# Performance work log

Measured on AMD Instinct MI355X. Metric: run time of the kernel, lower is better.

The kernel has to match this reference:

```python
import jax, jax.numpy as jnp
import numpy as np

T, B, V, E, H, L = 128, 32, 50000, 512, 512, 2


def _lstm_layer(x, h0, c0, Wih, Whh, bih, bhh):
    # x: [T, B, in]; torch gate order i, f, g, o
    def step(carry, xt):
        h, c = carry
        gates = xt @ Wih.T + bih + h @ Whh.T + bhh  # [B, 4H]
        i, f, g, o = jnp.split(gates, 4, axis=-1)
        c = jax.nn.sigmoid(f) * c + jax.nn.sigmoid(i) * jnp.tanh(g)
        h = jax.nn.sigmoid(o) * jnp.tanh(c)
        return (h, c), h
    (h, c), ys = jax.lax.scan(step, (h0, c0), x)
    return ys, h, c


def setup_inputs() -> dict:
    key = jax.random.key(0)
    ks = jax.random.split(key, 12)
    s = 0.02
    return {
        'word': jax.random.randint(ks[0], (B,), 0, V),
        'seq': jax.random.randint(ks[1], (T, B), 0, V),
        'emb': jax.random.normal(ks[2], (V, E), jnp.float32) * s,
        'w2h_W': jax.random.normal(ks[3], (H, E), jnp.float32) * s,
        'w2h_b': jnp.zeros((H,), jnp.float32),
        'Wih0': jax.random.normal(ks[4], (4 * H, E), jnp.float32) * s,
        'Whh0': jax.random.normal(ks[5], (4 * H, H), jnp.float32) * s,
        'bih0': jnp.zeros((4 * H,), jnp.float32),
        'bhh0': jnp.zeros((4 * H,), jnp.float32),
        'Wih1': jax.random.normal(ks[6], (4 * H, H), jnp.float32) * s,
        'Whh1': jax.random.normal(ks[7], (4 * H, H), jnp.float32) * s,
        'bih1': jnp.zeros((4 * H,), jnp.float32),
        'bhh1': jnp.zeros((4 * H,), jnp.float32),
        'dec_W': jax.random.normal(ks[8], (V, H), jnp.float32) * s,
        'dec_b': jnp.zeros((V,), jnp.float32),
    }


def reference(word, seq, emb, w2h_W, w2h_b, Wih0, Whh0, bih0, bhh0,
              Wih1, Whh1, bih1, bhh1, dec_W, dec_b):
    word_emb = emb[word]                       # [B, E]
    seq_emb = emb[seq]                         # [T, B, E] (dropouts are 0/eval)
    # init_hidden: c0 = word2hidden(word_emb) expanded to all layers, h0 = 0
    c0 = word_emb @ w2h_W.T + w2h_b            # [B, H]
    h0 = jnp.zeros_like(c0)
    # 2-layer LSTM; stepping all layers per timestep == running layers sequentially
    y0, h_f0, c_f0 = _lstm_layer(seq_emb, h0, c0, Wih0, Whh0, bih0, bhh0)
    y1, h_f1, c_f1 = _lstm_layer(y0, h0, c0, Wih1, Whh1, bih1, bhh1)
    out = y1.reshape(T * B, H)                 # [T*B, H]
    decoded = out @ dec_W.T + dec_b            # [T*B, V]
    h_final = jnp.stack([h_f0, h_f1], axis=0)  # [L, B, H]
    c_final = jnp.stack([c_f0, c_f1], axis=0)
    return decoded, h_final, c_final
```

## Files before the change

kernel.cpp:

```cpp
#include <hip/hip_runtime.h>
#include <hip/hip_bf16.h>
#include <cstdint>

#define T_STEPS 128
#define BATCH   32
#define VOCAB   50000
#define EDIM    512
#define HDIM    512
#define GDIM    2048
#define MROWS   4096
#define VPAD    50048

typedef short bf16x8 __attribute__((ext_vector_type(8)));
typedef float f32x4  __attribute__((ext_vector_type(4)));
typedef unsigned short us4 __attribute__((ext_vector_type(4)));
typedef unsigned short us8 __attribute__((ext_vector_type(8)));

__device__ __forceinline__ float sigmoidf_(float x) { return 1.0f / (1.0f + expf(-x)); }

__device__ __forceinline__ unsigned short f2bf(float f) {
    unsigned int u = __float_as_uint(f);
    u = (u + 0x7fffu + ((u >> 16) & 1u)) >> 16;
    return (unsigned short)u;
}


__global__ __launch_bounds__(256) void conv_decw(const float* __restrict__ src,
                                                 unsigned short* __restrict__ dst) {
    long i = ((long)blockIdx.x * 256 + threadIdx.x) * 8;
    if (i >= (long)VPAD * EDIM) return;
    long row = i >> 9;
    us8 v;
    if (row < VOCAB) {
        float4 a = *(const float4*)(src + i);
        float4 b = *(const float4*)(src + i + 4);
        v[0] = f2bf(a.x); v[1] = f2bf(a.y); v[2] = f2bf(a.z); v[3] = f2bf(a.w);
        v[4] = f2bf(b.x); v[5] = f2bf(b.y); v[6] = f2bf(b.z); v[7] = f2bf(b.w);
    } else {
        v = (us8)0;
    }
    *(us8*)(dst + i) = v;
}

__global__ __launch_bounds__(64) void pack_conv(const float* __restrict__ src,
                                                unsigned short* __restrict__ dst) {
    const int n = blockIdx.x;
    const int orig = (n & 3) * 512 + (n >> 2);
    const int k = threadIdx.x * 8;
    const float* s = src + (long)orig * 512 + k;
    float4 a = *(const float4*)s;
    float4 b = *(const float4*)(s + 4);
    us8 v;
    v[0] = f2bf(a.x); v[1] = f2bf(a.y); v[2] = f2bf(a.z); v[3] = f2bf(a.w);
    v[4] = f2bf(b.x); v[5] = f2bf(b.y); v[6] = f2bf(b.z); v[7] = f2bf(b.w);
    *(us8*)(dst + (long)n * 512 + k) = v;
}

__global__ __launch_bounds__(256) void pack_bias(const float* __restrict__ bih0,
                                                 const float* __restrict__ bhh0,
                                                 const float* __restrict__ bih1,
                                                 const float* __restrict__ bhh1,
                                                 float* __restrict__ b0p,
                                                 float* __restrict__ b1p) {
    const int n = blockIdx.x * 256 + threadIdx.x;
    const int orig = (n & 3) * 512 + (n >> 2);
    b0p[n] = bih0[orig] + bhh0[orig];
    b1p[n] = bih1[orig] + bhh1[orig];
}

__global__ __launch_bounds__(256) void gather_x(const int* __restrict__ seq,
                                                const float* __restrict__ emb,
                                                unsigned short* __restrict__ Xbf) {
    long i = ((long)blockIdx.x * 256 + threadIdx.x) * 4;
    if (i >= (long)MROWS * EDIM) return;
    int r   = (int)(i >> 9);
    int col = (int)(i & 511);
    const float* er = emb + (long)seq[r] * EDIM + col;
    float4 e = *(const float4*)er;
    us4 v;
    v[0] = f2bf(e.x); v[1] = f2bf(e.y); v[2] = f2bf(e.z); v[3] = f2bf(e.w);
    *(us4*)(Xbf + i) = v;
}

__global__ __launch_bounds__(256) void init_c0(const int* __restrict__ word,
                                               const float* __restrict__ emb,
                                               const float* __restrict__ w2hW,
                                               const float* __restrict__ w2hb,
                                               float* __restrict__ c0s, float* __restrict__ c1s,
                                               unsigned short* __restrict__ h0A,
                                               unsigned short* __restrict__ h1A) {
    const int idx = blockIdx.x * 256 + threadIdx.x;
    const int b = idx >> 9, hh = idx & 511;
    const float* er = emb + (long)word[b] * EDIM;
    const float* wr = w2hW + (long)hh * EDIM;
    float acc = w2hb[hh];
    #pragma unroll 4
    for (int k = 0; k < EDIM; k += 4) {
        float4 e4 = *(const float4*)(er + k);
        float4 w4 = *(const float4*)(wr + k);
        acc += e4.x * w4.x + e4.y * w4.y + e4.z * w4.z + e4.w * w4.w;
    }
    c0s[idx] = acc;
    c1s[idx] = acc;
    h0A[idx] = 0;
    h1A[idx] = 0;
}

__global__ __launch_bounds__(256) void gemm_bt128(const unsigned short* __restrict__ A,
                                                  const unsigned short* __restrict__ Bt,
                                                  float* __restrict__ C,
                                                  const float* __restrict__ bias1,
                                                  const float* __restrict__ bias2,
                                                  int K, int Nreal, long ldc, int ntn,
                                                  int ntstore) {
    __shared__ __align__(16) unsigned short As[128 * 64];
    __shared__ __align__(16) unsigned short Bs[128 * 64];
    const int tid  = threadIdx.x;
    const long m0  = (long)(blockIdx.x / ntn) * 128;
    const long n0  = (long)(blockIdx.x % ntn) * 128;
    const int lane = tid & 63;
    const int wave = tid >> 6;
    const int wr = wave >> 1, wc = wave & 1;
    const int fr = lane & 15, fq = lane >> 4;

    f32x4 acc[4][4];
    #pragma unroll
    for (int i = 0; i < 4; ++i)
        #pragma unroll
        for (int j = 0; j < 4; ++j) acc[i][j] = (f32x4)0.0f;

    const int srow = tid >> 3;
    const int scol = (tid & 7) * 8;

    for (int kt = 0; kt < K; kt += 64) {
        #pragma unroll
        for (int i = 0; i < 4; ++i) {
            const unsigned short* ga = A  + (m0 + i * 32 + srow) * K + kt + scol;
            const unsigned short* gb = Bt + (n0 + i * 32 + srow) * K + kt + scol;
            __builtin_amdgcn_global_load_lds((const __attribute__((address_space(1))) void*)ga,
                                             (__attribute__((address_space(3))) void*)(As + i * 2048 + tid * 8),
                                             16, 0, 0);
            __builtin_amdgcn_global_load_lds((const __attribute__((address_space(1))) void*)gb,
                                             (__attribute__((address_space(3))) void*)(Bs + i * 2048 + tid * 8),
                                             16, 0, 0);
        }
        asm volatile("s_waitcnt vmcnt(0)" ::: "memory");
        __syncthreads();
        #pragma unroll
        for (int ks = 0; ks < 64; ks += 32) {
            bf16x8 af[4], bfr[4];
            #pragma unroll
            for (int mi = 0; mi < 4; ++mi)
                af[mi] = *(const bf16x8*)&As[(wr * 64 + mi * 16 + fr) * 64 + ks + fq * 8];
            #pragma unroll
            for (int ni = 0; ni < 4; ++ni)
                bfr[ni] = *(const bf16x8*)&Bs[(wc * 64 + ni * 16 + fr) * 64 + ks + fq * 8];
            #pragma unroll
            for (int mi = 0; mi < 4; ++mi)
                #pragma unroll
                for (int ni = 0; ni < 4; ++ni)
                    acc[mi][ni] = __builtin_amdgcn_mfma_f32_16x16x32_bf16(af[mi], bfr[ni], acc[mi][ni], 0, 0, 0);
        }
        __syncthreads();
    }

    #pragma unroll
    for (int mi = 0; mi < 4; ++mi) {
        const long row = m0 + wr * 64 + mi * 16 + fq * 4;
        #pragma unroll
        for (int ni = 0; ni < 4; ++ni) {
            const long col = n0 + wc * 64 + ni * 16 + fr;
            if (col < Nreal) {
                float bs = (bias1 ? bias1[col] : 0.0f) + (bias2 ? bias2[col] : 0.0f);
                #pragma unroll
                for (int r = 0; r < 4; ++r) {
                    float v = acc[mi][ni][r] + bs;
                    float* p = &C[(row + r) * ldc + col];
                    if (ntstore) __builtin_nontemporal_store(v, p);
                    else *p = v;
                }
            }
        }
    }
}

__global__ __launch_bounds__(512) void lstm_step2(
        const float* __restrict__ G0,
        const unsigned short* __restrict__ Whh0p,
        const unsigned short* __restrict__ Wih1p,
        const unsigned short* __restrict__ Whh1p,
        const float* __restrict__ b1p,
        unsigned short* __restrict__ y0bf,
        unsigned short* __restrict__ y1bf,
        unsigned short* __restrict__ h0A, unsigned short* __restrict__ h0B,
        float* __restrict__ c0s,
        unsigned short* __restrict__ h1A, unsigned short* __restrict__ h1B,
        float* __restrict__ c1s,
        float* __restrict__ hf,
        int t) {
    __shared__ float part[8][32][32];
    int bid = blockIdx.x;
    const int tid  = threadIdx.x;
    const int wv   = tid >> 6, lane = tid & 63;
    const int fr   = lane & 15, fq = lane >> 4;

    int layer, tt, cg;
    if (bid < 64) { layer = 0; tt = t;     if (tt >= T_STEPS) return; cg = bid; }
    else          { layer = 1; tt = t - 1; if (tt < 0) return;       cg = bid - 64; }

    const unsigned short* hin;
    unsigned short* hout;
    float* cs;
    if (layer == 0) { hin = (tt & 1) ? h0B : h0A; hout = (tt & 1) ? h0A : h0B; cs = c0s; }
    else            { hin = (tt & 1) ? h1B : h1A; hout = (tt & 1) ? h1A : h1B; cs = c1s; }

    const int n_base = cg * 32;

    f32x4 acc[2][2];
    acc[0][0] = (f32x4)0.0f; acc[0][1] = (f32x4)0.0f;
    acc[1][0] = (f32x4)0.0f; acc[1][1] = (f32x4)0.0f;

    if (layer == 0) {
        const int kbase = wv * 64;
        const unsigned short* A0 = hin + fr * 512 + kbase + fq * 8;
        const unsigned short* A1 = A0 + 16 * 512;
        const unsigned short* B0 = Whh0p + (long)(n_base + fr) * 512 + kbase + fq * 8;
        const unsigned short* B1 = B0 + 16 * 512;
        #pragma unroll
        for (int i = 0; i < 2; ++i) {
            bf16x8 a0 = *(const bf16x8*)(A0 + i * 32);
            bf16x8 a1 = *(const bf16x8*)(A1 + i * 32);
            bf16x8 b0 = *(const bf16x8*)(B0 + i * 32);
            bf16x8 b1 = *(const bf16x8*)(B1 + i * 32);
            acc[0][0] = __builtin_amdgcn_mfma_f32_16x16x32_bf16(a0, b0, acc[0][0], 0, 0, 0);
            acc[0][1] = __builtin_amdgcn_mfma_f32_16x16x32_bf16(a0, b1, acc[0][1], 0, 0, 0);
            acc[1][0] = __builtin_amdgcn_mfma_f32_16x16x32_bf16(a1, b0, acc[1][0], 0, 0, 0);
            acc[1][1] = __builtin_amdgcn_mfma_f32_16x16x32_bf16(a1, b1, acc[1][1], 0, 0, 0);
        }
    } else {
        const unsigned short* Aop = (wv < 4) ? (y0bf + (long)tt * (BATCH * HDIM)) : hin;
        const unsigned short* Bop = (wv < 4) ? Wih1p : Whh1p;
        const int kbase = (wv & 3) * 128;
        const unsigned short* A0 = Aop + fr * 512 + kbase + fq * 8;
        const unsigned short* A1 = A0 + 16 * 512;
        const unsigned short* B0 = Bop + (long)(n_base + fr) * 512 + kbase + fq * 8;
        const unsigned short* B1 = B0 + 16 * 512;
        #pragma unroll
        for (int i = 0; i < 4; ++i) {
            bf16x8 a0 = *(const bf16x8*)(A0 + i * 32);
            bf16x8 a1 = *(const bf16x8*)(A1 + i * 32);
            bf16x8 b0 = *(const bf16x8*)(B0 + i * 32);
            bf16x8 b1 = *(const bf16x8*)(B1 + i * 32);
            acc[0][0] = __builtin_amdgcn_mfma_f32_16x16x32_bf16(a0, b0, acc[0][0], 0, 0, 0);
            acc[0][1] = __builtin_amdgcn_mfma_f32_16x16x32_bf16(a0, b1, acc[0][1], 0, 0, 0);
            acc[1][0] = __builtin_amdgcn_mfma_f32_16x16x32_bf16(a1, b0, acc[1][0], 0, 0, 0);
            acc[1][1] = __builtin_amdgcn_mfma_f32_16x16x32_bf16(a1, b1, acc[1][1], 0, 0, 0);
        }
    }

    #pragma unroll
    for (int mi = 0; mi < 2; ++mi)
        #pragma unroll
        for (int ni = 0; ni < 2; ++ni)
            #pragma unroll
            for (int r = 0; r < 4; ++r)
                part[wv][mi * 16 + fq * 4 + r][ni * 16 + fr] = acc[mi][ni][r];
    __syncthreads();

    if (tid < 256) {
        const int b = tid >> 3, u = tid & 7;
        float4 g4 = *(const float4*)&part[0][b][u * 4];
        #pragma unroll
        for (int w = 1; w < 8; ++w) {
            float4 p4 = *(const float4*)&part[w][b][u * 4];
            g4.x += p4.x; g4.y += p4.y; g4.z += p4.z; g4.w += p4.w;
        }
        float4 ad;
        if (layer == 0) ad = *(const float4*)(G0 + ((long)tt * BATCH + b) * GDIM + n_base + u * 4);
        else            ad = *(const float4*)(b1p + n_base + u * 4);
        const float vi = g4.x + ad.x, vf = g4.y + ad.y;
        const float vg = g4.z + ad.z, vo = g4.w + ad.w;
        const int si = b * HDIM + (n_base >> 2) + u;
        float c = sigmoidf_(vf) * cs[si] + sigmoidf_(vi) * tanhf(vg);
        float h = sigmoidf_(vo) * tanhf(c);
        cs[si] = c;
        const unsigned short hb = f2bf(h);
        hout[si] = hb;
        if (layer == 0) y0bf[(long)tt * (BATCH * HDIM) + si] = hb;
        else            y1bf[(long)tt * (BATCH * HDIM) + si] = hb;
        if (tt == T_STEPS - 1) hf[layer * (BATCH * HDIM) + si] = h;
    }
}

__global__ __launch_bounds__(256) void finalize_states(const float* __restrict__ hf,
                                                       const float* __restrict__ c0s,
                                                       const float* __restrict__ c1s,
                                                       float* __restrict__ out) {
    const int idx = blockIdx.x * 256 + threadIdx.x;
    const long base = (long)MROWS * VOCAB;
    float v;
    if (idx < 32768)      v = hf[idx];
    else if (idx < 49152) v = c0s[idx - 32768];
    else                  v = c1s[idx - 49152];
    out[base + idx] = v;
}

extern "C" void kernel_launch(void* const* d_in, const int* in_sizes, int n_in,
                              void* d_out, int out_size, void* d_ws, size_t ws_size,
                              hipStream_t stream) {
    const int*   word  = (const int*)d_in[0];
    const int*   seq   = (const int*)d_in[1];
    const float* emb   = (const float*)d_in[2];
    const float* w2hW  = (const float*)d_in[3];
    const float* w2hb  = (const float*)d_in[4];
    const float* Wih0  = (const float*)d_in[5];
    const float* Whh0  = (const float*)d_in[6];
    const float* bih0  = (const float*)d_in[7];
    const float* bhh0  = (const float*)d_in[8];
    const float* Wih1  = (const float*)d_in[9];
    const float* Whh1  = (const float*)d_in[10];
    const float* bih1  = (const float*)d_in[11];
    const float* bhh1  = (const float*)d_in[12];
    const float* dec_W = (const float*)d_in[13];
    const float* dec_b = (const float*)d_in[14];
    float* out = (float*)d_out;

    char* ws = (char*)d_ws;
    size_t off = 0;
    float*          G0    = (float*)(ws + off);          off += (size_t)MROWS * GDIM * 4;
    unsigned short* Xbf   = (unsigned short*)(ws + off); off += (size_t)MROWS * EDIM * 2;
    unsigned short* Wih0p = (unsigned short*)(ws + off); off += (size_t)GDIM  * EDIM * 2;
    unsigned short* Whh0p = (unsigned short*)(ws + off); off += (size_t)GDIM  * HDIM * 2;
    unsigned short* Wih1p = (unsigned short*)(ws + off); off += (size_t)GDIM  * HDIM * 2;
    unsigned short* Whh1p = (unsigned short*)(ws + off); off += (size_t)GDIM  * HDIM * 2;
    unsigned short* decWb = (unsigned short*)(ws + off); off += (size_t)VPAD  * EDIM * 2;
    unsigned short* y0bf  = (unsigned short*)(ws + off); off += (size_t)MROWS * HDIM * 2;
    unsigned short* y1bf  = (unsigned short*)(ws + off); off += (size_t)MROWS * HDIM * 2;
    float* b0p = (float*)(ws + off); off += (size_t)GDIM * 4;
    float* b1p = (float*)(ws + off); off += (size_t)GDIM * 4;
    unsigned short* h0A = (unsigned short*)(ws + off); off += (size_t)BATCH * HDIM * 2;
    unsigned short* h0B = (unsigned short*)(ws + off); off += (size_t)BATCH * HDIM * 2;
    unsigned short* h1A = (unsigned short*)(ws + off); off += (size_t)BATCH * HDIM * 2;
    unsigned short* h1B = (unsigned short*)(ws + off); off += (size_t)BATCH * HDIM * 2;
    float* c0s = (float*)(ws + off); off += (size_t)BATCH * HDIM * 4;
    float* c1s = (float*)(ws + off); off += (size_t)BATCH * HDIM * 4;
    float* hf  = (float*)(ws + off); off += (size_t)2 * BATCH * HDIM * 4;

    conv_decw<<<12512, 256, 0, stream>>>(dec_W, decWb);
    pack_conv<<<2048, 64, 0, stream>>>(Wih0, Wih0p);
    pack_conv<<<2048, 64, 0, stream>>>(Whh0, Whh0p);
    pack_conv<<<2048, 64, 0, stream>>>(Wih1, Wih1p);
    pack_conv<<<2048, 64, 0, stream>>>(Whh1, Whh1p);
    pack_bias<<<8, 256, 0, stream>>>(bih0, bhh0, bih1, bhh1, b0p, b1p);
    gather_x<<<2048, 256, 0, stream>>>(seq, emb, Xbf);
    init_c0<<<64, 256, 0, stream>>>(word, emb, w2hW, w2hb, c0s, c1s, h0A, h1A);

    gemm_bt128<<<32 * 16, 256, 0, stream>>>(Xbf, Wih0p, G0, b0p, nullptr,
                                            512, GDIM, (long)GDIM, 16, 0);

    for (int t = 0; t <= T_STEPS; ++t)
        lstm_step2<<<128, 512, 0, stream>>>(G0, Whh0p, Wih1p, Whh1p, b1p,
                                            y0bf, y1bf, h0A, h0B, c0s,
                                            h1A, h1B, c1s, hf, t);

    gemm_bt128<<<32 * 391, 256, 0, stream>>>(y1bf, decWb, out, dec_b, nullptr,
                                             512, VOCAB, (long)VOCAB, 391, 1);

    finalize_states<<<256, 256, 0, stream>>>(hf, c0s, c1s, out);
}
```

Before: 1.463 ms.

## Replace per-timestep LSTM launches with a persistent kernel using atomic counters

The 129 per-timestep lstm_step2 launches are replaced by one persistent kernel of 128 blocks. Each block keeps its slice of the recurrent weights and its cell state in registers across all timesteps. Blocks sync through per-timestep global counters that are spin-waited on with atomics, and layer 1 trails layer 0 by polling layer 0's counter. This removes launch overhead and repeated weight loads. In exchange it depends on all 128 blocks being co-resident and adds spin-wait and fence latency on every step.

```diff
diff --git a/kernel.cpp b/kernel.cpp
--- a/kernel.cpp
+++ b/kernel.cpp
@@ -15,6 +15,8 @@
 typedef float f32x4  __attribute__((ext_vector_type(4)));
 typedef unsigned short us4 __attribute__((ext_vector_type(4)));
 typedef unsigned short us8 __attribute__((ext_vector_type(8)));
+
+#define MFMA16(a, b, c) __builtin_amdgcn_mfma_f32_16x16x32_bf16(a, b, c, 0, 0, 0)
 
 __device__ __forceinline__ float sigmoidf_(float x) { return 1.0f / (1.0f + expf(-x)); }
 
@@ -88,8 +90,15 @@
                                                const float* __restrict__ w2hb,
                                                float* __restrict__ c0s, float* __restrict__ c1s,
                                                unsigned short* __restrict__ h0A,
-                                               unsigned short* __restrict__ h1A) {
+                                               unsigned short* __restrict__ h1A,
+                                               int* __restrict__ cnt0, int* __restrict__ cnt1) {
     const int idx = blockIdx.x * 256 + threadIdx.x;
+    if (blockIdx.x == 0) {
+        if (threadIdx.x < T_STEPS) {
+            cnt0[threadIdx.x] = 0;
+            cnt1[threadIdx.x] = 0;
+        }
+    }
     const int b = idx >> 9, hh = idx & 511;
     const float* er = emb + (long)word[b] * EDIM;
     const float* wr = w2hW + (long)hh * EDIM;
@@ -159,7 +168,7 @@
             for (int mi = 0; mi < 4; ++mi)
                 #pragma unroll
                 for (int ni = 0; ni < 4; ++ni)
-                    acc[mi][ni] = __builtin_amdgcn_mfma_f32_16x16x32_bf16(af[mi], bfr[ni], acc[mi][ni], 0, 0, 0);
+                    acc[mi][ni] = MFMA16(af[mi], bfr[ni], acc[mi][ni]);
         }
         __syncthreads();
     }
@@ -184,7 +193,7 @@
     }
 }
 
-__global__ __launch_bounds__(512) void lstm_step2(
+__global__ __launch_bounds__(512, 1) void lstm_persist(
         const float* __restrict__ G0,
         const unsigned short* __restrict__ Whh0p,
         const unsigned short* __restrict__ Wih1p,
@@ -197,98 +206,169 @@
         unsigned short* __restrict__ h1A, unsigned short* __restrict__ h1B,
         float* __restrict__ c1s,
         float* __restrict__ hf,
-        int t) {
+        int* __restrict__ cnt0, int* __restrict__ cnt1) {
     __shared__ float part[8][32][32];
-    int bid = blockIdx.x;
-    const int tid  = threadIdx.x;
-    const int wv   = tid >> 6, lane = tid & 63;
-    const int fr   = lane & 15, fq = lane >> 4;
-
-    int layer, tt, cg;
-    if (bid < 64) { layer = 0; tt = t;     if (tt >= T_STEPS) return; cg = bid; }
-    else          { layer = 1; tt = t - 1; if (tt < 0) return;       cg = bid - 64; }
-
-    const unsigned short* hin;
-    unsigned short* hout;
-    float* cs;
-    if (layer == 0) { hin = (tt & 1) ? h0B : h0A; hout = (tt & 1) ? h0A : h0B; cs = c0s; }
-    else            { hin = (tt & 1) ? h1B : h1A; hout = (tt & 1) ? h1A : h1B; cs = c1s; }
-
-    const int n_base = cg * 32;
-
-    f32x4 acc[2][2];
-    acc[0][0] = (f32x4)0.0f; acc[0][1] = (f32x4)0.0f;
-    acc[1][0] = (f32x4)0.0f; acc[1][1] = (f32x4)0.0f;
-
-    if (layer == 0) {
-        const int kbase = wv * 64;
-        const unsigned short* A0 = hin + fr * 512 + kbase + fq * 8;
-        const unsigned short* A1 = A0 + 16 * 512;
-        const unsigned short* B0 = Whh0p + (long)(n_base + fr) * 512 + kbase + fq * 8;
-        const unsigned short* B1 = B0 + 16 * 512;
+    const int tid = threadIdx.x;
+    const int wv = tid >> 6, lane = tid & 63;
+    const int fr = lane & 15, fq = lane >> 4;
+    const int koff = fq * 8;
+    const int bid = blockIdx.x;
+    const int pb = tid >> 3, pu = tid & 7;
+
+    if (bid < 64) {
+        const int n_base = bid * 32;
+        const int kbase  = wv * 64;
+        const unsigned short* W0 = Whh0p + (long)(n_base + fr) * 512 + kbase + koff;
+        const unsigned short* W1 = W0 + 16 * 512;
+        const bf16x8 w00 = *(const bf16x8*)(W0);
+        const bf16x8 w01 = *(const bf16x8*)(W0 + 32);
+        const bf16x8 w10 = *(const bf16x8*)(W1);
+        const bf16x8 w11 = *(const bf16x8*)(W1 + 32);
+        const int si = pb * HDIM + bid * 8 + pu;
+        float creg = 0.0f;
+        if (tid < 256) creg = c0s[si];
+
+        for (int t = 0; t < T_STEPS; ++t) {
+            const unsigned short* hin = (t & 1) ? h0B : h0A;
+            unsigned short* hout      = (t & 1) ? h0A : h0B;
+            if (t > 0) {
+                if (tid == 0)
+                    while (__hip_atomic_load(cnt0 + t - 1, __ATOMIC_RELAXED,
+                                             __HIP_MEMORY_SCOPE_AGENT) < 64)
+                        __builtin_amdgcn_s_sleep(1);
+                __syncthreads();
+                __threadfence();
+            }
+            const unsigned short* A0 = hin + fr * 512 + kbase + koff;
+            const unsigned short* A1 = A0 + 16 * 512;
+            const bf16x8 a00 = *(const bf16x8*)(A0);
+            const bf16x8 a01 = *(const bf16x8*)(A0 + 32);
+            const bf16x8 a10 = *(const bf16x8*)(A1);
+            const bf16x8 a11 = *(const bf16x8*)(A1 + 32);
+            float4 ad;
+            if (tid < 256)
+                ad = *(const float4*)(G0 + ((long)t * BATCH + pb) * GDIM + n_base + pu * 4);
+            f32x4 acc00 = (f32x4)0.0f, acc01 = (f32x4)0.0f;
+            f32x4 acc10 = (f32x4)0.0f, acc11 = (f32x4)0.0f;
+            acc00 = MFMA16(a00, w00, acc00); acc00 = MFMA16(a01, w01, acc00);
+            acc01 = MFMA16(a00, w10, acc01); acc01 = MFMA16(a01, w11, acc01);
+            acc10 = MFMA16(a10, w00, acc10); acc10 = MFMA16(a11, w01, acc10);
+            acc11 = MFMA16(a10, w10, acc11); acc11 = MFMA16(a11, w11, acc11);
+            #pragma unroll
+            for (int r = 0; r < 4; ++r) {
+                part[wv][fq * 4 + r][fr]           = acc00[r];
+                part[wv][fq * 4 + r][16 + fr]      = acc01[r];
+                part[wv][16 + fq * 4 + r][fr]      = acc10[r];
+                part[wv][16 + fq * 4 + r][16 + fr] = acc11[r];
+            }
+            __syncthreads();
+            if (tid < 256) {
+                float4 g4 = *(const float4*)&part[0][pb][pu * 4];
+                #pragma unroll
+                for (int w = 1; w < 8; ++w) {
+                    float4 p4 = *(const float4*)&part[w][pb][pu * 4];
+                    g4.x += p4.x; g4.y += p4.y; g4.z += p4.z; g4.w += p4.w;
+                }
+                const float vi = g4.x + ad.x, vf = g4.y + ad.y;
+                const float vg = g4.z + ad.z, vo = g4.w + ad.w;
+                float c = sigmoidf_(vf) * creg + sigmoidf_(vi) * tanhf(vg);
+                float h = sigmoidf_(vo) * tanhf(c);
+                creg = c;
+                const unsigned short hb = f2bf(h);
+                hout[si] = hb;
+                y0bf[(long)t * (BATCH * HDIM) + si] = hb;
+                if (t == T_STEPS - 1) { hf[si] = h; c0s[si] = c; }
+            }
+            __threadfence();
+            __syncthreads();
+            if (tid == 0)
+                __hip_atomic_fetch_add(cnt0 + t, 1, __ATOMIC_RELEASE,
+                                       __HIP_MEMORY_SCOPE_AGENT);
+        }
+    } else {
+        const int cg = bid - 64;
+        const int n_base = cg * 32;
+        const int kbase  = (wv & 3) * 128;
+        const unsigned short* Bop = (wv < 4) ? Wih1p : Whh1p;
+        const unsigned short* WB0 = Bop + (long)(n_base + fr) * 512 + kbase + koff;
+        const unsigned short* WB1 = WB0 + 16 * 512;
+        bf16x8 wb0[4], wb1[4];
         #pragma unroll
-        for (int i = 0; i < 2; ++i) {
-            bf16x8 a0 = *(const bf16x8*)(A0 + i * 32);
-            bf16x8 a1 = *(const bf16x8*)(A1 + i * 32);
-            bf16x8 b0 = *(const bf16x8*)(B0 + i * 32);
-            bf16x8 b1 = *(const bf16x8*)(B1 + i * 32);
-            acc[0][0] = __builtin_amdgcn_mfma_f32_16x16x32_bf16(a0, b0, acc[0][0], 0, 0, 0);
-            acc[0][1] = __builtin_amdgcn_mfma_f32_16x16x32_bf16(a0, b1, acc[0][1], 0, 0, 0);
-            acc[1][0] = __builtin_amdgcn_mfma_f32_16x16x32_bf16(a1, b0, acc[1][0], 0, 0, 0);
-            acc[1][1] = __builtin_amdgcn_mfma_f32_16x16x32_bf16(a1, b1, acc[1][1], 0, 0, 0);
-        }
-    } else {
-        const unsigned short* Aop = (wv < 4) ? (y0bf + (long)tt * (BATCH * HDIM)) : hin;
-        const unsigned short* Bop = (wv < 4) ? Wih1p : Whh1p;
-        const int kbase = (wv & 3) * 128;
-        const unsigned short* A0 = Aop + fr * 512 + kbase + fq * 8;
-        const unsigned short* A1 = A0 + 16 * 512;
-        const unsigned short* B0 = Bop + (long)(n_base + fr) * 512 + kbase + fq * 8;
-        const unsigned short* B1 = B0 + 16 * 512;
-        #pragma unroll
-        for (int i = 0; i < 4; ++i) {
-            bf16x8 a0 = *(const bf16x8*)(A0 + i * 32);
-            bf16x8 a1 = *(const bf16x8*)(A1 + i * 32);
-            bf16x8 b0 = *(const bf16x8*)(B0 + i * 32);
-            bf16x8 b1 = *(const bf16x8*)(B1 + i * 32);
-            acc[0][0] = __builtin_amdgcn_mfma_f32_16x16x32_bf16(a0, b0, acc[0][0], 0, 0, 0);
-            acc[0][1] = __builtin_amdgcn_mfma_f32_16x16x32_bf16(a0, b1, acc[0][1], 0, 0, 0);
-            acc[1][0] = __builtin_amdgcn_mfma_f32_16x16x32_bf16(a1, b0, acc[1][0], 0, 0, 0);
-            acc[1][1] = __builtin_amdgcn_mfma_f32_16x16x32_bf16(a1, b1, acc[1][1], 0, 0, 0);
-        }
-    }
-
-    #pragma unroll
-    for (int mi = 0; mi < 2; ++mi)
-        #pragma unroll
-        for (int ni = 0; ni < 2; ++ni)
-            #pragma unroll
-            for (int r = 0; r < 4; ++r)
-                part[wv][mi * 16 + fq * 4 + r][ni * 16 + fr] = acc[mi][ni][r];
-    __syncthreads();
-
-    if (tid < 256) {
-        const int b = tid >> 3, u = tid & 7;
-        float4 g4 = *(const float4*)&part[0][b][u * 4];
-        #pragma unroll
-        for (int w = 1; w < 8; ++w) {
-            float4 p4 = *(const float4*)&part[w][b][u * 4];
-            g4.x += p4.x; g4.y += p4.y; g4.z += p4.z; g4.w += p4.w;
-        }
-        float4 ad;
-        if (layer == 0) ad = *(const float4*)(G0 + ((long)tt * BATCH + b) * GDIM + n_base + u * 4);
-        else            ad = *(const float4*)(b1p + n_base + u * 4);
-        const float vi = g4.x + ad.x, vf = g4.y + ad.y;
-        const float vg = g4.z + ad.z, vo = g4.w + ad.w;
-        const int si = b * HDIM + (n_base >> 2) + u;
-        float c = sigmoidf_(vf) * cs[si] + sigmoidf_(vi) * tanhf(vg);
-        float h = sigmoidf_(vo) * tanhf(c);
-        cs[si] = c;
-        const unsigned short hb = f2bf(h);
-        hout[si] = hb;
-        if (layer == 0) y0bf[(long)tt * (BATCH * HDIM) + si] = hb;
-        else            y1bf[(long)tt * (BATCH * HDIM) + si] = hb;
-        if (tt == T_STEPS - 1) hf[layer * (BATCH * HDIM) + si] = h;
+        for (int kt = 0; kt < 4; ++kt) {
+            wb0[kt] = *(const bf16x8*)(WB0 + kt * 32);
+            wb1[kt] = *(const bf16x8*)(WB1 + kt * 32);
+        }
+        const int si = pb * HDIM + cg * 8 + pu;
+        float creg = 0.0f;
+        float4 bb = make_float4(0.f, 0.f, 0.f, 0.f);
+        if (tid < 256) {
+            creg = c1s[si];
+            bb = *(const float4*)(b1p + n_base + pu * 4);
+        }
+
+        for (int t = 0; t < T_STEPS; ++t) {
+            const unsigned short* hin = (t & 1) ? h1B : h1A;
+            unsigned short* hout      = (t & 1) ? h1A : h1B;
+            if (tid == 0) {
+                while (__hip_atomic_load(cnt0 + t, __ATOMIC_RELAXED,
+                                         __HIP_MEMORY_SCOPE_AGENT) < 64)
+                    __builtin_amdgcn_s_sleep(1);
+                if (t > 0)
+                    while (__hip_atomic_load(cnt1 + t - 1, __ATOMIC_RELAXED,
+                                             __HIP_MEMORY_SCOPE_AGENT) < 64)
+                        __builtin_amdgcn_s_sleep(1);
+            }
+            __syncthreads();
+            __threadfence();
+            const unsigned short* Aop = (wv < 4) ? (y0bf + (long)t * (BATCH * HDIM)) : hin;
+            const unsigned short* A0 = Aop + fr * 512 + kbase + koff;
+            const unsigned short* A1 = A0 + 16 * 512;
+            bf16x8 a0[4], a1[4];
+            #pragma unroll
+            for (int kt = 0; kt < 4; ++kt) {
+                a0[kt] = *(const bf16x8*)(A0 + kt * 32);
+                a1[kt] = *(const bf16x8*)(A1 + kt * 32);
+            }
+            f32x4 acc00 = (f32x4)0.0f, acc01 = (f32x4)0.0f;
+            f32x4 acc10 = (f32x4)0.0f, acc11 = (f32x4)0.0f;
+            #pragma unroll
+            for (int kt = 0; kt < 4; ++kt) {
+                acc00 = MFMA16(a0[kt], wb0[kt], acc00);
+                acc01 = MFMA16(a0[kt], wb1[kt], acc01);
+                acc10 = MFMA16(a1[kt], wb0[kt], acc10);
+                acc11 = MFMA16(a1[kt], wb1[kt], acc11);
+            }
+            #pragma unroll
+            for (int r = 0; r < 4; ++r) {
+                part[wv][fq * 4 + r][fr]           = acc00[r];
+                part[wv][fq * 4 + r][16 + fr]      = acc01[r];
+                part[wv][16 + fq * 4 + r][fr]      = acc10[r];
+                part[wv][16 + fq * 4 + r][16 + fr] = acc11[r];
+            }
+            __syncthreads();
+            if (tid < 256) {
+                float4 g4 = *(const float4*)&part[0][pb][pu * 4];
+                #pragma unroll
+                for (int w = 1; w < 8; ++w) {
+                    float4 p4 = *(const float4*)&part[w][pb][pu * 4];
+                    g4.x += p4.x; g4.y += p4.y; g4.z += p4.z; g4.w += p4.w;
+                }
+                const float vi = g4.x + bb.x, vf = g4.y + bb.y;
+                const float vg = g4.z + bb.z, vo = g4.w + bb.w;
+                float c = sigmoidf_(vf) * creg + sigmoidf_(vi) * tanhf(vg);
+                float h = sigmoidf_(vo) * tanhf(c);
+                creg = c;
+                const unsigned short hb = f2bf(h);
+                hout[si] = hb;
+                y1bf[(long)t * (BATCH * HDIM) + si] = hb;
+                if (t == T_STEPS - 1) { hf[BATCH * HDIM + si] = h; c1s[si] = c; }
+            }
+            __threadfence();
+            __syncthreads();
+            if (tid == 0)
+                __hip_atomic_fetch_add(cnt1 + t, 1, __ATOMIC_RELEASE,
+                                       __HIP_MEMORY_SCOPE_AGENT);
+        }
     }
 }
 
@@ -345,6 +425,8 @@
     float* c0s = (float*)(ws + off); off += (size_t)BATCH * HDIM * 4;
     float* c1s = (float*)(ws + off); off += (size_t)BATCH * HDIM * 4;
     float* hf  = (float*)(ws + off); off += (size_t)2 * BATCH * HDIM * 4;
+    int*   cnt0 = (int*)(ws + off); off += (size_t)T_STEPS * 4;
+    int*   cnt1 = (int*)(ws + off); off += (size_t)T_STEPS * 4;
 
     conv_decw<<<12512, 256, 0, stream>>>(dec_W, decWb);
     pack_conv<<<2048, 64, 0, stream>>>(Wih0, Wih0p);
@@ -353,15 +435,15 @@
     pack_conv<<<2048, 64, 0, stream>>>(Whh1, Whh1p);
     pack_bias<<<8, 256, 0, stream>>>(bih0, bhh0, bih1, bhh1, b0p, b1p);
     gather_x<<<2048, 256, 0, stream>>>(seq, emb, Xbf);
-    init_c0<<<64, 256, 0, stream>>>(word, emb, w2hW, w2hb, c0s, c1s, h0A, h1A);
+    init_c0<<<64, 256, 0, stream>>>(word, emb, w2hW, w2hb, c0s, c1s, h0A, h1A,
+                                    cnt0, cnt1);
 
     gemm_bt128<<<32 * 16, 256, 0, stream>>>(Xbf, Wih0p, G0, b0p, nullptr,
                                             512, GDIM, (long)GDIM, 16, 0);
 
-    for (int t = 0; t <= T_STEPS; ++t)
-        lstm_step2<<<128, 512, 0, stream>>>(G0, Whh0p, Wih1p, Whh1p, b1p,
-                                            y0bf, y1bf, h0A, h0B, c0s,
-                                            h1A, h1B, c1s, hf, t);
+    lstm_persist<<<128, 512, 0, stream>>>(G0, Whh0p, Wih1p, Whh1p, b1p,
+                                          y0bf, y1bf, h0A, h0B, c0s,
+                                          h1A, h1B, c1s, hf, cnt0, cnt1);
 
     gemm_bt128<<<32 * 391, 256, 0, stream>>>(y1bf, decWb, out, dec_b, nullptr,
                                              512, VOCAB, (long)VOCAB, 391, 1);
```

After: 5.510 ms. 277% more time.
